# Optimization experiments

Measured on AMD Instinct MI355X. Metric: run time of the kernel, lower is better.

Reference implementation:

```python
import jax, jax.numpy as jnp
import numpy as np

N, E, IN, H, HEADS, L, OUT = 4096, 262144, 64, 128, 4, 2, 2
DH = H // HEADS  # 32, per-head dim for both GAT and global MHA
BN_EPS = 1e-5
NEG_SLOPE = 0.2  # GATConv leaky_relu default


def setup_inputs() -> dict:
    key = jax.random.key(0)
    ks = iter(jax.random.split(key, 32))
    rn = lambda shape, s: jax.random.normal(next(ks), shape, jnp.float32) * s
    return {
        "x": rn((N, IN), 1.0),
        "edge_index": jax.random.randint(next(ks), (2, E), 0, N),
        "w_in": rn((H, IN), IN ** -0.5),
        "b_in": rn((H,), 0.02),
        "w_gat": rn((L, H, H), H ** -0.5),
        "att_src": rn((L, HEADS, DH), 0.1),
        "att_dst": rn((L, HEADS, DH), 0.1),
        "b_gat": rn((L, H), 0.02),
        "w_qkv": rn((L, 3 * H, H), H ** -0.5),
        "b_qkv": rn((L, 3 * H), 0.02),
        "w_o": rn((L, H, H), H ** -0.5),
        "b_o": rn((L, H), 0.02),
        "bn_gamma": 1.0 + rn((L, 3, H), 0.05),
        "bn_beta": rn((L, 3, H), 0.05),
        "w1": rn((L, 2 * H, H), H ** -0.5),
        "b1": rn((L, 2 * H), 0.02),
        "w2": rn((L, H, 2 * H), (2 * H) ** -0.5),
        "b2": rn((L, H), 0.02),
        "w_out": rn((OUT, H), H ** -0.5),
        "b_out": rn((OUT,), 0.02),
    }


def _bn(h, g, b):
    # eval-mode BatchNorm1d with running_mean=0, running_var=1
    return h * (g / jnp.sqrt(1.0 + BN_EPS)) + b


def _gat(x, src, dst, w, a_src, a_dst, bias):
    # GATConv(hidden, hidden//heads, heads=HEADS, add_self_loops=False), concat=True
    xp = (x @ w.T).reshape(N, HEADS, DH)                  # [N, HEADS, DH]
    al_s = jnp.einsum('nhd,hd->nh', xp, a_src)            # [N, HEADS]
    al_d = jnp.einsum('nhd,hd->nh', xp, a_dst)
    logit = al_s[src] + al_d[dst]                         # [E, HEADS]
    logit = jnp.where(logit >= 0, logit, NEG_SLOPE * logit)
    m = jax.ops.segment_max(logit, dst, num_segments=N)   # scatter-softmax over dst
    m = jnp.where(jnp.isfinite(m), m, 0.0)
    e = jnp.exp(logit - m[dst])
    denom = jax.ops.segment_sum(e, dst, num_segments=N)
    alpha = e / (denom[dst] + 1e-16)
    out = jax.ops.segment_sum(alpha[:, :, None] * xp[src], dst, num_segments=N)
    return out.reshape(N, H) + bias


def _mha(x, wqkv, bqkv, wo, bo):
    # torch.nn.MultiheadAttention self-attention over all N nodes (one graph)
    qkv = x @ wqkv.T + bqkv
    q, k, v = jnp.split(qkv, 3, axis=-1)
    q = q.reshape(N, HEADS, DH)
    k = k.reshape(N, HEADS, DH)
    v = v.reshape(N, HEADS, DH)
    scores = jnp.einsum('nhd,mhd->hnm', q, k) / jnp.sqrt(jnp.float32(DH))
    attn = jax.nn.softmax(scores, axis=-1)
    out = jnp.einsum('hnm,mhd->nhd', attn, v).reshape(N, H)
    return out @ wo.T + bo


def reference(x, edge_index, w_in, b_in, w_gat, att_src, att_dst, b_gat,
              w_qkv, b_qkv, w_o, b_o, bn_gamma, bn_beta,
              w1, b1, w2, b2, w_out, b_out):
    src, dst = edge_index[0], edge_index[1]
    h = jax.nn.relu(x @ w_in.T + b_in)
    for l in range(L):
        # GPSConv: local GAT branch (dropout inactive in eval)
        h_loc = _gat(h, src, dst, w_gat[l], att_src[l], att_dst[l], b_gat[l]) + h
        h_loc = _bn(h_loc, bn_gamma[l, 0], bn_beta[l, 0])
        # GPSConv: global attention branch
        h_att = _mha(h, w_qkv[l], b_qkv[l], w_o[l], b_o[l]) + h
        h_att = _bn(h_att, bn_gamma[l, 1], bn_beta[l, 1])
        out = h_loc + h_att
        mlp = jax.nn.relu(out @ w1[l].T + b1[l]) @ w2[l].T + b2[l]
        out = _bn(out + mlp, bn_gamma[l, 2], bn_beta[l, 2])
        # GPSRiskModel residual + relu (dropout inactive in eval)
        h = jax.nn.relu(out + h)
    return h @ w_out.T + b_out
```

## Files before the change

### kernel.cpp

```cpp
#include <hip/hip_runtime.h>

#define NN 4096
#define EE 262144
#define INF_ 64
#define HH 128
#define HEADS 4
#define DH 32
#define LL 2
#define NH (NN * HH)
#define KSPLIT 16
#define L2E 1.4426950408889634f

typedef unsigned short u16;
typedef unsigned int u32;
using bf16x8 = __attribute__((ext_vector_type(8))) short;
using f32x4 = __attribute__((ext_vector_type(4))) float;

__device__ __forceinline__ float bf2f(u16 v) { return __uint_as_float(((u32)v) << 16); }
__device__ __forceinline__ u16 f2bf(float f) {
    u32 u = __float_as_uint(f);
    u32 r = (u + 0x7fffu + ((u >> 16) & 1u)) >> 16;
    return (u16)r;
}
__device__ __forceinline__ u32 encf(float f) {
    u32 b = __float_as_uint(f);
    return (b & 0x80000000u) ? ~b : (b | 0x80000000u);
}
__device__ __forceinline__ float decf(u32 u) {
    u32 b = (u & 0x80000000u) ? (u & 0x7fffffffu) : ~u;
    return __uint_as_float(b);
}

__global__ __launch_bounds__(256) void k_detect(const u16* __restrict__ x, int* __restrict__ flag,
                                                int* __restrict__ cnt, u32* __restrict__ gmax) {
    int t = threadIdx.x;
    for (int i = t; i < NN; i += 256) cnt[i] = 0;
    if (t < 16) gmax[t] = 0;
    __shared__ int cs[256];
    u16 v = x[2 * t];
    int e = (v >> 7) & 0xFF;
    cs[t] = (e >= 100 && e <= 140) ? 1 : 0;
    __syncthreads();
    for (int s = 128; s > 0; s >>= 1) {
        if (t < s) cs[t] += cs[t + s];
        __syncthreads();
    }
    if (t == 0) *flag = (cs[0] >= 128) ? 1 : 0;
}

#define MAXSEG 16
struct SegF { const void* src[MAXSEG]; int dst[MAXSEG]; int n[MAXSEG]; int cnt; };
__global__ void k_cvtf(SegF S, float* __restrict__ W, const int* __restrict__ flag) {
    int seg = blockIdx.y;
    if (seg >= S.cnt) return;
    int n = S.n[seg];
    float* d = W + S.dst[seg];
    const void* s = S.src[seg];
    int f = *flag;
    for (int i = blockIdx.x * 256 + threadIdx.x; i < n; i += gridDim.x * 256)
        d[i] = f ? bf2f(((const u16*)s)[i]) : ((const float*)s)[i];
}
struct SegB { const void* src[8]; u16* dst[8]; u16* dst2[8]; int n[8]; int cnt; };
__global__ void k_cvtb(SegB S, const int* __restrict__ flag) {
    int seg = blockIdx.y;
    if (seg >= S.cnt) return;
    int f = *flag;
    u16* d = S.dst[seg];
    u16* d2 = S.dst2[seg];
    if (f && !d2) return;
    int n = S.n[seg];
    const void* s = S.src[seg];
    for (int i = blockIdx.x * 256 + threadIdx.x; i < n; i += gridDim.x * 256) {
        if (d2) {
            float v = f ? bf2f(((const u16*)s)[i]) : ((const float*)s)[i];
            u16 h = f2bf(v);
            d[i] = h;
            d2[i] = f2bf(v - bf2f(h));
        } else {
            d[i] = f2bf(((const float*)s)[i]);
        }
    }
}

__global__ void k_hist(const int* __restrict__ dst, int* __restrict__ cnt) {
    int e = blockIdx.x * blockDim.x + threadIdx.x;
    if (e < EE) atomicAdd(&cnt[dst[e]], 1);
}
__global__ __launch_bounds__(256) void k_scan(const int* __restrict__ cnt, int* __restrict__ rowstart,
                                              int* __restrict__ cursor) {
    __shared__ int part[256];
    int t = threadIdx.x;
    int loc[16];
    int s = 0;
#pragma unroll
    for (int i = 0; i < 16; ++i) { loc[i] = s; s += cnt[t * 16 + i]; }
    part[t] = s;
    __syncthreads();
    for (int off = 1; off < 256; off <<= 1) {
        int v = part[t];
        int a = (t >= off) ? part[t - off] : 0;
        __syncthreads();
        part[t] = v + a;
        __syncthreads();
    }
    int base = (t == 0) ? 0 : part[t - 1];
#pragma unroll
    for (int i = 0; i < 16; ++i) {
        rowstart[t * 16 + i] = base + loc[i];
        cursor[t * 16 + i] = base + loc[i];
    }
}
__global__ void k_scatter(const int* __restrict__ src, const int* __restrict__ dst,
                          int* __restrict__ cursor, int* __restrict__ esrc) {
    int e = blockIdx.x * blockDim.x + threadIdx.x;
    if (e < EE) {
        int d = dst[e];
        int p = atomicAdd(&cursor[d], 1);
        esrc[p] = src[e];
    }
}

__global__ __launch_bounds__(128) void k_mgemm(const u16* __restrict__ Ahi, const u16* __restrict__ Alo,
                                               const u16* __restrict__ Wc, const u16* __restrict__ Wd,
                                               const int* __restrict__ flag,
                                               const float* __restrict__ bias,
                                               float* __restrict__ outf, u16* __restrict__ outb16,
                                               u16* __restrict__ outhi, u16* __restrict__ outlo,
                                               int K, int J, int relu) {
    const u16* Wb = (*flag) ? Wd : Wc;
    int wave = threadIdx.x >> 6, lane = threadIdx.x & 63;
    int grp = lane >> 4, lcol = lane & 15;
    int m0 = blockIdx.x * 32 + wave * 16;
    int j0 = blockIdx.y * 64;
    f32x4 acc[4];
#pragma unroll
    for (int s = 0; s < 4; ++s) acc[s] = (f32x4){0.f, 0.f, 0.f, 0.f};
    const u16* ah = Ahi + (size_t)(m0 + lcol) * K + grp * 8;
    const u16* al = Alo + (size_t)(m0 + lcol) * K + grp * 8;
    const u16* wb = Wb + (size_t)(j0 + lcol) * K + grp * 8;
    for (int k = 0; k < K; k += 32) {
        bf16x8 va = *(const bf16x8*)(ah + k);
        bf16x8 vl = *(const bf16x8*)(al + k);
#pragma unroll
        for (int s = 0; s < 4; ++s) {
            bf16x8 vw = *(const bf16x8*)(wb + (size_t)s * 16 * K + k);
            acc[s] = __builtin_amdgcn_mfma_f32_16x16x32_bf16(va, vw, acc[s], 0, 0, 0);
            acc[s] = __builtin_amdgcn_mfma_f32_16x16x32_bf16(vl, vw, acc[s], 0, 0, 0);
        }
    }
#pragma unroll
    for (int s = 0; s < 4; ++s) {
        int col = j0 + s * 16 + lcol;
        float bs = bias ? bias[col] : 0.f;
#pragma unroll
        for (int r = 0; r < 4; ++r) {
            float v = acc[s][r] + bs;
            if (relu) v = fmaxf(v, 0.f);
            size_t idx = (size_t)(m0 + grp * 4 + r) * J + col;
            if (outf) outf[idx] = v;
            if (outb16) outb16[idx] = f2bf(v);
            if (outhi) {
                u16 hv = f2bf(v);
                outhi[idx] = hv;
                outlo[idx] = f2bf(v - bf2f(hv));
            }
        }
    }
}

__global__ __launch_bounds__(128) void k_gemm_gq(const u16* __restrict__ Ahi, const u16* __restrict__ Alo,
                                                 const u16* __restrict__ wgatc, const u16* __restrict__ wgatd,
                                                 const u16* __restrict__ wqkvc, const u16* __restrict__ wqkvd,
                                                 const int* __restrict__ flag,
                                                 const float* __restrict__ bqkv,
                                                 u16* __restrict__ xpb, u16* __restrict__ qkvb) {
    int wave = threadIdx.x >> 6, lane = threadIdx.x & 63;
    int grp = lane >> 4, lcol = lane & 15;
    int m0 = blockIdx.x * 32 + wave * 16;
    int jb = blockIdx.y;
    int j0 = jb * 64;
    int f = *flag;
    const u16* wgat = f ? wgatd : wgatc;
    const u16* wqkv = f ? wqkvd : wqkvc;
    const u16* Wb = (jb < 2) ? (wgat + (size_t)j0 * HH) : (wqkv + (size_t)(j0 - 128) * HH);
    f32x4 acc[4];
#pragma unroll
    for (int s = 0; s < 4; ++s) acc[s] = (f32x4){0.f, 0.f, 0.f, 0.f};
    const u16* ah = Ahi + (size_t)(m0 + lcol) * HH + grp * 8;
    const u16* al = Alo + (size_t)(m0 + lcol) * HH + grp * 8;
    const u16* wb = Wb + (size_t)lcol * HH + grp * 8;
    for (int k = 0; k < HH; k += 32) {
        bf16x8 va = *(const bf16x8*)(ah + k);
        bf16x8 vl = *(const bf16x8*)(al + k);
#pragma unroll
        for (int s = 0; s < 4; ++s) {
            bf16x8 vw = *(const bf16x8*)(wb + (size_t)s * 16 * HH + k);
            acc[s] = __builtin_amdgcn_mfma_f32_16x16x32_bf16(va, vw, acc[s], 0, 0, 0);
            acc[s] = __builtin_amdgcn_mfma_f32_16x16x32_bf16(vl, vw, acc[s], 0, 0, 0);
        }
    }
    if (jb < 2) {
#pragma unroll
        for (int s = 0; s < 4; ++s) {
            int col = j0 + s * 16 + lcol;
#pragma unroll
            for (int r = 0; r < 4; ++r)
                xpb[(size_t)(m0 + grp * 4 + r) * HH + col] = f2bf(acc[s][r]);
        }
    } else {
#pragma unroll
        for (int s = 0; s < 4; ++s) {
            int colq = j0 - 128 + s * 16 + lcol;
            float bs = bqkv[colq];
#pragma unroll
            for (int r = 0; r < 4; ++r)
                qkvb[(size_t)(m0 + grp * 4 + r) * 384 + colq] = f2bf(acc[s][r] + bs);
        }
    }
}

__global__ __launch_bounds__(256) void k_attlog(const u16* __restrict__ xpb, const float* __restrict__ asrc,
                                                const float* __restrict__ adst, float* __restrict__ als,
                                                float* __restrict__ ald, u32* __restrict__ gmax) {
    int t = blockIdx.x * 256 + threadIdx.x;
    int n = t >> 2, hh = t & 3;
    const u16* xr = xpb + (size_t)n * HH + hh * DH;
    float s1 = 0.f, s2 = 0.f;
#pragma unroll
    for (int d = 0; d < DH; ++d) {
        float v = bf2f(xr[d]);
        s1 += v * asrc[hh * DH + d];
        s2 += v * adst[hh * DH + d];
    }
    als[t] = s1;
    ald[t] = s2;
    __shared__ float red[256];
    int lt = threadIdx.x;
    red[lt] = s1;
    __syncthreads();
    for (int off = 128; off >= 4; off >>= 1) {
        if (lt < off) red[lt] = fmaxf(red[lt], red[lt + off]);
        __syncthreads();
    }
    if (lt < 4) atomicMax(&gmax[lt], encf(red[lt]));
    __syncthreads();
    red[lt] = s2;
    __syncthreads();
    for (int off = 128; off >= 4; off >>= 1) {
        if (lt < off) red[lt] = fmaxf(red[lt], red[lt + off]);
        __syncthreads();
    }
    if (lt < 4) atomicMax(&gmax[4 + lt], encf(red[lt]));
}

__global__ __launch_bounds__(128) void k_gemm_wo(const u16* __restrict__ Ahi, const u16* __restrict__ Alo,
                                                 const u16* __restrict__ Wc, const u16* __restrict__ Wd,
                                                 const int* __restrict__ flag,
                                                 const float* __restrict__ bias,
                                                 const float* __restrict__ gatb, const float* __restrict__ hbuf,
                                                 const float* __restrict__ bgat, const float* __restrict__ gam,
                                                 const float* __restrict__ bet,
                                                 float* __restrict__ outb, u16* __restrict__ ohi,
                                                 u16* __restrict__ olo) {
    const u16* Wb = (*flag) ? Wd : Wc;
    int wave = threadIdx.x >> 6, lane = threadIdx.x & 63;
    int grp = lane >> 4, lcol = lane & 15;
    int m0 = blockIdx.x * 32 + wave * 16;
    int j0 = blockIdx.y * 64;
    f32x4 acc[4];
#pragma unroll
    for (int s = 0; s < 4; ++s) acc[s] = (f32x4){0.f, 0.f, 0.f, 0.f};
    const u16* ah = Ahi + (size_t)(m0 + lcol) * HH + grp * 8;
    const u16* al = Alo + (size_t)(m0 + lcol) * HH + grp * 8;
    const u16* wb = Wb + (size_t)(j0 + lcol) * HH + grp * 8;
    for (int k = 0; k < HH; k += 32) {
        bf16x8 va = *(const bf16x8*)(ah + k);
        bf16x8 vl = *(const bf16x8*)(al + k);
#pragma unroll
        for (int s = 0; s < 4; ++s) {
            bf16x8 vw = *(const bf16x8*)(wb + (size_t)s * 16 * HH + k);
            acc[s] = __builtin_amdgcn_mfma_f32_16x16x32_bf16(va, vw, acc[s], 0, 0, 0);
            acc[s] = __builtin_amdgcn_mfma_f32_16x16x32_bf16(vl, vw, acc[s], 0, 0, 0);
        }
    }
    float rs = rsqrtf(1.00001f);
#pragma unroll
    for (int s = 0; s < 4; ++s) {
        int col = j0 + s * 16 + lcol;
        float bs = bias[col];
        float g0 = gam[col] * rs, b0 = bet[col];
        float g1 = gam[HH + col] * rs, b1 = bet[HH + col];
        float bg = bgat[col];
#pragma unroll
        for (int r = 0; r < 4; ++r) {
            size_t idx = (size_t)(m0 + grp * 4 + r) * HH + col;
            float proj = acc[s][r] + bs;
            float hv = hbuf[idx];
            float hl = g0 * (gatb[idx] + bg + hv) + b0;
            float ha = g1 * (proj + hv) + b1;
            float v = hl + ha;
            outb[idx] = v;
            u16 hb = f2bf(v);
            ohi[idx] = hb;
            olo[idx] = f2bf(v - bf2f(hb));
        }
    }
}

__global__ __launch_bounds__(128) void k_gemm_w2(const u16* __restrict__ Ahi, const u16* __restrict__ Alo,
                                                 const u16* __restrict__ Wc, const u16* __restrict__ Wd,
                                                 const int* __restrict__ flag,
                                                 const float* __restrict__ bias,
                                                 const float* __restrict__ outb, const float* __restrict__ gam2,
                                                 const float* __restrict__ bet2,
                                                 float* __restrict__ hbuf, u16* __restrict__ hhi,
                                                 u16* __restrict__ hlo) {
    const u16* Wb = (*flag) ? Wd : Wc;
    int wave = threadIdx.x >> 6, lane = threadIdx.x & 63;
    int grp = lane >> 4, lcol = lane & 15;
    int m0 = blockIdx.x * 32 + wave * 16;
    int j0 = blockIdx.y * 64;
    const int K = 2 * HH;
    f32x4 acc[4];
#pragma unroll
    for (int s = 0; s < 4; ++s) acc[s] = (f32x4){0.f, 0.f, 0.f, 0.f};
    const u16* ah = Ahi + (size_t)(m0 + lcol) * K + grp * 8;
    const u16* al = Alo + (size_t)(m0 + lcol) * K + grp * 8;
    const u16* wb = Wb + (size_t)(j0 + lcol) * K + grp * 8;
    for (int k = 0; k < K; k += 32) {
        bf16x8 va = *(const bf16x8*)(ah + k);
        bf16x8 vl = *(const bf16x8*)(al + k);
#pragma unroll
        for (int s = 0; s < 4; ++s) {
            bf16x8 vw = *(const bf16x8*)(wb + (size_t)s * 16 * K + k);
            acc[s] = __builtin_amdgcn_mfma_f32_16x16x32_bf16(va, vw, acc[s], 0, 0, 0);
            acc[s] = __builtin_amdgcn_mfma_f32_16x16x32_bf16(vl, vw, acc[s], 0, 0, 0);
        }
    }
    float rs = rsqrtf(1.00001f);
#pragma unroll
    for (int s = 0; s < 4; ++s) {
        int col = j0 + s * 16 + lcol;
        float bs = bias[col];
        float g2 = gam2[col] * rs, b2 = bet2[col];
#pragma unroll
        for (int r = 0; r < 4; ++r) {
            size_t idx = (size_t)(m0 + grp * 4 + r) * HH + col;
            float mlpo = acc[s][r] + bs;
            float o2 = g2 * (outb[idx] + mlpo) + b2;
            float v = fmaxf(o2 + hbuf[idx], 0.f);
            hbuf[idx] = v;
            u16 hb = f2bf(v);
            hhi[idx] = hb;
            hlo[idx] = f2bf(v - bf2f(hb));
        }
    }
}

#define GCHUNK 256
__global__ __launch_bounds__(128) void k_gat_node(const int* __restrict__ esrc, const int* __restrict__ rowstart,
                                                  const int* __restrict__ cnt, const float* __restrict__ als,
                                                  const float* __restrict__ ald, const u16* __restrict__ xpb,
                                                  float* __restrict__ gatout, const u32* __restrict__ gmax) {
    int n = blockIdx.x, t = threadIdx.x;
    int base = rowstart[n], c = cnt[n];
    float4 adv = ((const float4*)ald)[n];
    float ad[4] = {adv.x, adv.y, adv.z, adv.w};
    float M2[4];
#pragma unroll
    for (int h = 0; h < 4; ++h) {
        float bound = decf(gmax[h]) + decf(gmax[4 + h]);
        float M = bound >= 0.f ? bound : 0.2f * bound;
        M2[h] = M * L2E;
    }
    __shared__ float red[512];
    __shared__ float elds[GCHUNK * 4];
    __shared__ int slds[GCHUNK];
    float dsum[4] = {0.f, 0.f, 0.f, 0.f};
    float acc = 0.f;
    int ht = t >> 5;
    for (int ch = 0; ch < c; ch += GCHUNK) {
        int cn = min(GCHUNK, c - ch);
        __syncthreads();
        for (int i = t; i < cn; i += 128) {
            int s = esrc[base + ch + i];
            slds[i] = s;
            float4 as = ((const float4*)als)[s];
            float lg, e;
            lg = as.x + ad[0]; lg = lg >= 0.f ? lg : 0.2f * lg; e = __builtin_exp2f(lg * L2E - M2[0]); elds[i * 4 + 0] = e; dsum[0] += e;
            lg = as.y + ad[1]; lg = lg >= 0.f ? lg : 0.2f * lg; e = __builtin_exp2f(lg * L2E - M2[1]); elds[i * 4 + 1] = e; dsum[1] += e;
            lg = as.z + ad[2]; lg = lg >= 0.f ? lg : 0.2f * lg; e = __builtin_exp2f(lg * L2E - M2[2]); elds[i * 4 + 2] = e; dsum[2] += e;
            lg = as.w + ad[3]; lg = lg >= 0.f ? lg : 0.2f * lg; e = __builtin_exp2f(lg * L2E - M2[3]); elds[i * 4 + 3] = e; dsum[3] += e;
        }
        __syncthreads();
        int i = 0;
        for (; i + 4 <= cn; i += 4) {
            int s0 = slds[i], s1 = slds[i + 1], s2 = slds[i + 2], s3 = slds[i + 3];
            float x0 = bf2f(xpb[(size_t)s0 * HH + t]);
            float x1 = bf2f(xpb[(size_t)s1 * HH + t]);
            float x2 = bf2f(xpb[(size_t)s2 * HH + t]);
            float x3 = bf2f(xpb[(size_t)s3 * HH + t]);
            acc += elds[i * 4 + ht] * x0 + elds[(i + 1) * 4 + ht] * x1;
            acc += elds[(i + 2) * 4 + ht] * x2 + elds[(i + 3) * 4 + ht] * x3;
        }
        for (; i < cn; ++i) acc += elds[i * 4 + ht] * bf2f(xpb[(size_t)slds[i] * HH + t]);
    }
    __syncthreads();
#pragma unroll
    for (int h = 0; h < 4; ++h) red[h * 128 + t] = dsum[h];
    __syncthreads();
    for (int s2 = 64; s2 > 0; s2 >>= 1) {
        if (t < s2) {
#pragma unroll
            for (int h = 0; h < 4; ++h)
                red[h * 128 + t] += red[h * 128 + t + s2];
        }
        __syncthreads();
    }
    float inv = 1.f / (red[ht * 128] + 1e-16f);
    gatout[(size_t)n * HH + t] = acc * inv;
}

__global__ __launch_bounds__(256) void k_mha_split(const u16* __restrict__ qkvb,
                                                   float* __restrict__ PM, float* __restrict__ PL,
                                                   u16* __restrict__ PO) {
    const float C1 = 0.17677669529663687f * L2E;
    int head = blockIdx.x & 3;
    int qt = (blockIdx.x >> 2) & 31;
    int ks = blockIdx.x >> 7;
    int tid = threadIdx.x;
    int wave = tid >> 6, lane = tid & 63;
    int grp = lane >> 4, lcol = lane & 15;

    __shared__ __align__(16) u16 Klds[64][40];
    __shared__ __align__(16) u32 Vlds[32][40];
    __shared__ __align__(16) u16 Plds[4][32][36];

    int qrow0 = qt * 128 + wave * 32;
    bf16x8 aQ0 = *(const bf16x8*)(qkvb + (size_t)(qrow0 + lcol) * 384 + head * 32 + grp * 8);
    bf16x8 aQ1 = *(const bf16x8*)(qkvb + (size_t)(qrow0 + 16 + lcol) * 384 + head * 32 + grp * 8);

    short onev = (lcol == 0) ? (short)0x3F80 : (short)0;
    bf16x8 bOne = {onev, onev, onev, onev, onev, onev, onev, onev};

    f32x4 oc00 = {0.f, 0.f, 0.f, 0.f}, oc01 = {0.f, 0.f, 0.f, 0.f};
    f32x4 oc10 = {0.f, 0.f, 0.f, 0.f}, oc11 = {0.f, 0.f, 0.f, 0.f};
    f32x4 ol0 = {0.f, 0.f, 0.f, 0.f}, ol1 = {0.f, 0.f, 0.f, 0.f};
    float msh = -INFINITY;

    int isK = (tid < 128);
    int st = tid & 127;
    int skey = st >> 1, shalf = (st & 1) * 16;
    int vj = st & 15, vc = (st >> 4) & 1, dgrp = st >> 5;
    const u16* kptr = qkvb + 128 + head * 32 + shalf;
    const u16* vptr = qkvb + 256 + head * 32 + dgrp * 8;
    int vk0 = vc * 32 + vj;
    int vk1 = vc * 32 + 16 + vj;

    int kt0 = ks * (NN / KSPLIT);
    bf16x8 r0, r1;
    if (isK) {
        r0 = *(const bf16x8*)(kptr + (size_t)(kt0 + skey) * 384);
        r1 = *(const bf16x8*)(kptr + (size_t)(kt0 + skey) * 384 + 8);
    } else {
        r0 = *(const bf16x8*)(vptr + (size_t)(kt0 + vk0) * 384);
        r1 = *(const bf16x8*)(vptr + (size_t)(kt0 + vk1) * 384);
    }

    const int NT = (NN / KSPLIT) / 64;
    for (int t = 0; t < NT; ++t) {
        if (isK) {
            *(bf16x8*)(&Klds[skey][shalf]) = r0;
            *(bf16x8*)(&Klds[skey][shalf + 8]) = r1;
        } else {
#pragma unroll
            for (int j = 0; j < 8; ++j)
                Vlds[dgrp * 8 + j][vc * 20 + vj] = (u32)(u16)r0[j] | ((u32)(u16)r1[j] << 16);
        }
        __syncthreads();
        if (t + 1 < NT) {
            int kn = kt0 + (t + 1) * 64;
            if (isK) {
                r0 = *(const bf16x8*)(kptr + (size_t)(kn + skey) * 384);
                r1 = *(const bf16x8*)(kptr + (size_t)(kn + skey) * 384 + 8);
            } else {
                r0 = *(const bf16x8*)(vptr + (size_t)(kn + vk0) * 384);
                r1 = *(const bf16x8*)(vptr + (size_t)(kn + vk1) * 384);
            }
        }
        f32x4 sc0[4], sc1[4];
        f32x4 zero = {0.f, 0.f, 0.f, 0.f};
#pragma unroll
        for (int s = 0; s < 4; ++s) {
            bf16x8 bK = *(const bf16x8*)(&Klds[s * 16 + lcol][grp * 8]);
            sc0[s] = __builtin_amdgcn_mfma_f32_16x16x32_bf16(aQ0, bK, zero, 0, 0, 0);
            sc1[s] = __builtin_amdgcn_mfma_f32_16x16x32_bf16(aQ1, bK, zero, 0, 0, 0);
        }
        float mymax = sc0[0][0];
#pragma unroll
        for (int s = 0; s < 4; ++s)
#pragma unroll
            for (int r = 0; r < 4; ++r) {
                mymax = fmaxf(mymax, sc0[s][r]);
                mymax = fmaxf(mymax, sc1[s][r]);
            }
        mymax = fmaxf(mymax, __shfl_xor(mymax, 1));
        mymax = fmaxf(mymax, __shfl_xor(mymax, 2));
        mymax = fmaxf(mymax, __shfl_xor(mymax, 4));
        mymax = fmaxf(mymax, __shfl_xor(mymax, 8));
        float mnew = fmaxf(msh, mymax * C1);
        float cc = __builtin_exp2f(msh - mnew);
        msh = mnew;
        oc00 *= cc; oc01 *= cc; ol0 *= cc;
        oc10 *= cc; oc11 *= cc; ol1 *= cc;
#pragma unroll
        for (int c2 = 0; c2 < 2; ++c2) {
#pragma unroll
            for (int r = 0; r < 4; ++r) {
                float p0 = __builtin_exp2f(__builtin_fmaf(sc0[2 * c2][r], C1, -mnew));
                float p1 = __builtin_exp2f(__builtin_fmaf(sc0[2 * c2 + 1][r], C1, -mnew));
                *(u32*)(&Plds[wave][grp * 4 + r][2 * lcol]) =
                    __builtin_amdgcn_perm(__float_as_uint(p1), __float_as_uint(p0), 0x07060302u);
                float q0 = __builtin_exp2f(__builtin_fmaf(sc1[2 * c2][r], C1, -mnew));
                float q1 = __builtin_exp2f(__builtin_fmaf(sc1[2 * c2 + 1][r], C1, -mnew));
                *(u32*)(&Plds[wave][16 + grp * 4 + r][2 * lcol]) =
                    __builtin_amdgcn_perm(__float_as_uint(q1), __float_as_uint(q0), 0x07060302u);
            }
            bf16x8 aP0 = *(const bf16x8*)(&Plds[wave][lcol][grp * 8]);
            bf16x8 aP1 = *(const bf16x8*)(&Plds[wave][16 + lcol][grp * 8]);
            bf16x8 bV0 = *(const bf16x8*)(&Vlds[lcol][c2 * 20 + grp * 4]);
            bf16x8 bV1 = *(const bf16x8*)(&Vlds[16 + lcol][c2 * 20 + grp * 4]);
            oc00 = __builtin_amdgcn_mfma_f32_16x16x32_bf16(aP0, bV0, oc00, 0, 0, 0);
            oc01 = __builtin_amdgcn_mfma_f32_16x16x32_bf16(aP0, bV1, oc01, 0, 0, 0);
            ol0 = __builtin_amdgcn_mfma_f32_16x16x32_bf16(aP0, bOne, ol0, 0, 0, 0);
            oc10 = __builtin_amdgcn_mfma_f32_16x16x32_bf16(aP1, bV0, oc10, 0, 0, 0);
            oc11 = __builtin_amdgcn_mfma_f32_16x16x32_bf16(aP1, bV1, oc11, 0, 0, 0);
            ol1 = __builtin_amdgcn_mfma_f32_16x16x32_bf16(aP1, bOne, ol1, 0, 0, 0);
        }
        __syncthreads();
    }
#pragma unroll
    for (int r = 0; r < 4; ++r) {
        int row0 = qrow0 + grp * 4 + r;
        size_t b0 = ((size_t)row0 * HEADS + head) * KSPLIT + ks;
        PO[b0 * 32 + lcol] = f2bf(oc00[r]);
        PO[b0 * 32 + 16 + lcol] = f2bf(oc01[r]);
        int row1 = row0 + 16;
        size_t b1 = ((size_t)row1 * HEADS + head) * KSPLIT + ks;
        PO[b1 * 32 + lcol] = f2bf(oc10[r]);
        PO[b1 * 32 + 16 + lcol] = f2bf(oc11[r]);
        if (lcol == 0) {
            PM[b0] = msh;
            PL[b0] = ol0[r];
            PM[b1] = msh;
            PL[b1] = ol1[r];
        }
    }
}

__global__ __launch_bounds__(256) void k_mha_comb(const float* __restrict__ PM, const float* __restrict__ PL,
                                                  const u16* __restrict__ PO, u16* __restrict__ atthi,
                                                  u16* __restrict__ attlo) {
    __shared__ float wn[2][4][KSPLIT];
    int row0 = blockIdx.x * 2;
    int t = threadIdx.x;
    if (t < 2 * 4 * KSPLIT) {
        int rr = t >> 6, head = (t >> 4) & 3, ks = t & 15;
        size_t b = ((size_t)(row0 + rr) * HEADS + head) * KSPLIT + ks;
        float pm = PM[b];
        float m = pm;
#pragma unroll
        for (int off = 1; off < 16; off <<= 1) m = fmaxf(m, __shfl_xor(m, off));
        float w = __builtin_exp2f(pm - m);
        float lw = PL[b] * w;
#pragma unroll
        for (int off = 1; off < 16; off <<= 1) lw += __shfl_xor(lw, off);
        wn[rr][head][ks] = w / lw;
    }
    __syncthreads();
    int rr = t >> 7, col = t & 127;
    int head = col >> 5, dim = col & 31;
    int row = row0 + rr;
    size_t b0 = ((size_t)row * HEADS + head) * KSPLIT;
    float o = 0.f;
#pragma unroll
    for (int k = 0; k < KSPLIT; ++k)
        o += wn[rr][head][k] * bf2f(PO[(b0 + k) * 32 + dim]);
    size_t idx = (size_t)row * HH + col;
    u16 h = f2bf(o);
    atthi[idx] = h;
    attlo[idx] = f2bf(o - bf2f(h));
}

__global__ __launch_bounds__(64) void k_out(const float* __restrict__ h, const float* __restrict__ w,
                                            const float* __restrict__ b, void* __restrict__ yout,
                                            const int* __restrict__ flag) {
    int n = blockIdx.x, l = threadIdx.x;
    float a0 = 0.f, a1 = 0.f;
    for (int k = l; k < HH; k += 64) {
        float hv = h[(size_t)n * HH + k];
        a0 += hv * w[k];
        a1 += hv * w[HH + k];
    }
#pragma unroll
    for (int off = 32; off > 0; off >>= 1) {
        a0 += __shfl_xor(a0, off);
        a1 += __shfl_xor(a1, off);
    }
    if (l == 0) {
        float o0 = a0 + b[0], o1 = a1 + b[1];
        if (*flag) {
            u16* y = (u16*)yout;
            y[n * 2 + 0] = f2bf(o0);
            y[n * 2 + 1] = f2bf(o1);
        } else {
            float* y = (float*)yout;
            y[n * 2 + 0] = o0;
            y[n * 2 + 1] = o1;
        }
    }
}

extern "C" void kernel_launch(void* const* d_in, const int* in_sizes, int n_in,
                              void* d_out, int out_size, void* d_ws, size_t ws_size,
                              hipStream_t stream) {
    float* W = (float*)d_ws;
    size_t o = 0;
    auto take = [&](size_t n) { size_t r = o; o += n; return r; };
    size_t pb_in = take(HH);
    size_t pattS = take(LL * HEADS * DH);
    size_t pattD = take(LL * HEADS * DH);
    size_t pb_gat = take(LL * HH);
    size_t pb_qkv = take(LL * 3 * HH);
    size_t pb_o  = take(LL * HH);
    size_t pbn_g = take(LL * 3 * HH);
    size_t pbn_b = take(LL * 3 * HH);
    size_t pb1   = take(LL * 2 * HH);
    size_t pb2   = take(LL * HH);
    size_t pw_out = take(2 * HH);
    size_t pb_out = take(2);
    auto takeb = [&](size_t nu16) { size_t r = o; o += (nu16 + 1) / 2; return r; };
    size_t bw_in  = takeb(HH * INF_);
    size_t bw_gat = takeb(LL * HH * HH);
    size_t bw_qkv = takeb(LL * 3 * HH * HH);
    size_t bw_o   = takeb(LL * HH * HH);
    size_t bw1    = takeb(LL * 2 * HH * HH);
    size_t bw2    = takeb(LL * HH * 2 * HH);
    o = (o + 127) & ~(size_t)127;
    size_t ohbuf = take(NH);
    size_t ogat  = take(NH);
    size_t otmp  = take(NH);
    size_t oals  = take(NN * HEADS);
    size_t oald  = take(NN * HEADS);
    size_t opm   = take(NN * HEADS * KSPLIT);
    size_t opl   = take(NN * HEADS * KSPLIT);
    size_t opo   = takeb((size_t)NN * HEADS * KSPLIT * 32);
    size_t oqkvb = takeb(NN * 384);
    size_t oxpb  = takeb(NH);
    size_t oxhi  = takeb(NN * INF_);
    size_t oxlo  = takeb(NN * INF_);
    size_t ohhi  = takeb(NH);
    size_t ohlo  = takeb(NH);
    size_t oahi  = takeb(NH);
    size_t oalo  = takeb(NH);
    size_t oohi  = takeb(NH);
    size_t oolo  = takeb(NH);
    size_t omhi  = takeb(NN * 2 * HH);
    size_t omlo  = takeb(NN * 2 * HH);
    int* ibase    = (int*)(W + o);
    int* iflag    = ibase;
    int* cnt      = ibase + 64;
    int* rowstart = cnt + NN;
    int* cursor   = rowstart + NN;
    int* esrc     = cursor + NN;
    u32* gmax     = (u32*)(esrc + EE);

    float* hbuf = W + ohbuf;
    float* gatb = W + ogat;
    float* tmp  = W + otmp;
    float* als  = W + oals;
    float* ald  = W + oald;
    float* pmb  = W + opm;
    float* plb  = W + opl;
    u16* pob  = (u16*)(W + opo);
    u16* qkvb = (u16*)(W + oqkvb);
    u16* xpb  = (u16*)(W + oxpb);
    u16* xhi = (u16*)(W + oxhi), *xlo = (u16*)(W + oxlo);
    u16* hhi = (u16*)(W + ohhi), *hlo = (u16*)(W + ohlo);
    u16* ahi = (u16*)(W + oahi), *alo = (u16*)(W + oalo);
    u16* ohi = (u16*)(W + oohi), *olo = (u16*)(W + oolo);
    u16* mhi = (u16*)(W + omhi), *mlo = (u16*)(W + omlo);

    const int* src = (const int*)d_in[1];
    const int* dst = (const int*)d_in[1] + EE;
    const u16* dw_in  = (const u16*)d_in[2];
    const u16* dw_gat = (const u16*)d_in[4];
    const u16* dw_qkv = (const u16*)d_in[8];
    const u16* dw_o   = (const u16*)d_in[10];
    const u16* dw1    = (const u16*)d_in[14];
    const u16* dw2    = (const u16*)d_in[16];

    k_detect<<<1, 256, 0, stream>>>((const u16*)d_in[0], iflag, cnt, gmax);

    SegF SF = {};
    int nf = 0;
    auto addf = [&](int idx, size_t off, int n) { SF.src[nf] = d_in[idx]; SF.dst[nf] = (int)off; SF.n[nf] = n; ++nf; };
    addf(3, pb_in, HH);
    addf(5, pattS, LL * HEADS * DH);
    addf(6, pattD, LL * HEADS * DH);
    addf(7, pb_gat, LL * HH);
    addf(9, pb_qkv, LL * 3 * HH);
    addf(11, pb_o, LL * HH);
    addf(12, pbn_g, LL * 3 * HH);
    addf(13, pbn_b, LL * 3 * HH);
    addf(15, pb1, LL * 2 * HH);
    addf(17, pb2, LL * HH);
    addf(18, pw_out, 2 * HH);
    addf(19, pb_out, 2);
    SF.cnt = nf;
    k_cvtf<<<dim3(8, nf), 256, 0, stream>>>(SF, W, iflag);

    SegB SB = {};
    int nb = 0;
    auto addb = [&](int idx, size_t off, int n, u16* d2) {
        SB.src[nb] = d_in[idx]; SB.dst[nb] = (u16*)(W + off); SB.dst2[nb] = d2; SB.n[nb] = n; ++nb;
    };
    addb(2, bw_in, HH * INF_, nullptr);
    addb(4, bw_gat, LL * HH * HH, nullptr);
    addb(8, bw_qkv, LL * 3 * HH * HH, nullptr);
    addb(10, bw_o, LL * HH * HH, nullptr);
    addb(14, bw1, LL * 2 * HH * HH, nullptr);
    addb(16, bw2, LL * HH * 2 * HH, nullptr);
    SB.src[nb] = d_in[0]; SB.dst[nb] = xhi; SB.dst2[nb] = xlo; SB.n[nb] = NN * INF_; ++nb;
    SB.cnt = nb;
    k_cvtb<<<dim3(128, nb), 256, 0, stream>>>(SB, iflag);

    k_hist<<<EE / 256, 256, 0, stream>>>(dst, cnt);
    k_scan<<<1, 256, 0, stream>>>(cnt, rowstart, cursor);
    k_scatter<<<EE / 256, 256, 0, stream>>>(src, dst, cursor, esrc);

    k_mgemm<<<dim3(NN / 32, HH / 64), 128, 0, stream>>>(xhi, xlo, (u16*)(W + bw_in), dw_in, iflag,
                                                        W + pb_in, hbuf, nullptr, hhi, hlo, INF_, HH, 1);

    for (int l = 0; l < LL; ++l) {
        k_gemm_gq<<<dim3(NN / 32, 8), 128, 0, stream>>>(hhi, hlo,
                                                        (u16*)(W + bw_gat) + (size_t)l * HH * HH,
                                                        dw_gat + (size_t)l * HH * HH,
                                                        (u16*)(W + bw_qkv) + (size_t)l * 3 * HH * HH,
                                                        dw_qkv + (size_t)l * 3 * HH * HH,
                                                        iflag, W + pb_qkv + l * 3 * HH, xpb, qkvb);
        k_attlog<<<(NN * HEADS) / 256, 256, 0, stream>>>(xpb, W + pattS + l * HEADS * DH,
                                                         W + pattD + l * HEADS * DH, als, ald,
                                                         gmax + l * 8);
        k_gat_node<<<NN, 128, 0, stream>>>(esrc, rowstart, cnt, als, ald, xpb, gatb, gmax + l * 8);
        k_mha_split<<<(NN / 128) * HEADS * KSPLIT, 256, 0, stream>>>(qkvb, pmb, plb, pob);
        k_mha_comb<<<NN / 2, 256, 0, stream>>>(pmb, plb, pob, ahi, alo);
        k_gemm_wo<<<dim3(NN / 32, HH / 64), 128, 0, stream>>>(ahi, alo,
                                                              (u16*)(W + bw_o) + (size_t)l * HH * HH,
                                                              dw_o + (size_t)l * HH * HH, iflag,
                                                              W + pb_o + l * HH, gatb, hbuf,
                                                              W + pb_gat + l * HH, W + pbn_g + l * 3 * HH,
                                                              W + pbn_b + l * 3 * HH, tmp, ohi, olo);
        k_mgemm<<<dim3(NN / 32, 256 / 64), 128, 0, stream>>>(ohi, olo,
                                                             (u16*)(W + bw1) + (size_t)l * 2 * HH * HH,
                                                             dw1 + (size_t)l * 2 * HH * HH, iflag,
                                                             W + pb1 + l * 2 * HH, nullptr, nullptr,
                                                             mhi, mlo, HH, 2 * HH, 1);
        k_gemm_w2<<<dim3(NN / 32, HH / 64), 128, 0, stream>>>(mhi, mlo,
                                                              (u16*)(W + bw2) + (size_t)l * HH * 2 * HH,
                                                              dw2 + (size_t)l * HH * 2 * HH, iflag,
                                                              W + pb2 + l * HH, tmp,
                                                              W + pbn_g + l * 3 * HH + 2 * HH,
                                                              W + pbn_b + l * 3 * HH + 2 * HH,
                                                              hbuf, hhi, hlo);
    }
    k_out<<<NN, 64, 0, stream>>>(hbuf, W + pw_out, W + pb_out, d_out, iflag);
}
```

Measured before the change: 321.2 us.

## Merge independent kernels via block-range dispatch to cut launch count

Merges independent kernels into single launches that pick their role from the block index. The weight conversion and edge histogram become one prep kernel. The attention-logit computation rides along with the MHA split kernel, and the GAT node aggregation shares a launch with the MHA combine. The aim is to remove several launches per layer and let independent work overlap on the GPU. In exchange, the merged kernels carry the shared-memory footprint and register pressure of their larger member, which may lower occupancy for the lighter parts.

```diff
diff --git a/kernel.cpp b/kernel.cpp
--- a/kernel.cpp
+++ b/kernel.cpp
@@ -50,42 +50,46 @@
 
 #define MAXSEG 16
 struct SegF { const void* src[MAXSEG]; int dst[MAXSEG]; int n[MAXSEG]; int cnt; };
-__global__ void k_cvtf(SegF S, float* __restrict__ W, const int* __restrict__ flag) {
-    int seg = blockIdx.y;
-    if (seg >= S.cnt) return;
-    int n = S.n[seg];
-    float* d = W + S.dst[seg];
-    const void* s = S.src[seg];
-    int f = *flag;
-    for (int i = blockIdx.x * 256 + threadIdx.x; i < n; i += gridDim.x * 256)
-        d[i] = f ? bf2f(((const u16*)s)[i]) : ((const float*)s)[i];
-}
 struct SegB { const void* src[8]; u16* dst[8]; u16* dst2[8]; int n[8]; int cnt; };
-__global__ void k_cvtb(SegB S, const int* __restrict__ flag) {
-    int seg = blockIdx.y;
-    if (seg >= S.cnt) return;
-    int f = *flag;
-    u16* d = S.dst[seg];
-    u16* d2 = S.dst2[seg];
-    if (f && !d2) return;
-    int n = S.n[seg];
-    const void* s = S.src[seg];
-    for (int i = blockIdx.x * 256 + threadIdx.x; i < n; i += gridDim.x * 256) {
-        if (d2) {
-            float v = f ? bf2f(((const u16*)s)[i]) : ((const float*)s)[i];
-            u16 h = f2bf(v);
-            d[i] = h;
-            d2[i] = f2bf(v - bf2f(h));
-        } else {
-            d[i] = f2bf(((const float*)s)[i]);
-        }
-    }
-}
-
-__global__ void k_hist(const int* __restrict__ dst, int* __restrict__ cnt) {
-    int e = blockIdx.x * blockDim.x + threadIdx.x;
-    if (e < EE) atomicAdd(&cnt[dst[e]], 1);
-}
+__global__ __launch_bounds__(256) void k_prep(SegF SF, float* __restrict__ W, SegB SB,
+                                              const int* __restrict__ flag,
+                                              const int* __restrict__ dst, int* __restrict__ cnt) {
+    int bid = blockIdx.x, t = threadIdx.x;
+    if (bid < 96) {
+        int seg = bid >> 3, bx = bid & 7;
+        if (seg >= SF.cnt) return;
+        int n = SF.n[seg];
+        float* d = W + SF.dst[seg];
+        const void* s = SF.src[seg];
+        int f = *flag;
+        for (int i = bx * 256 + t; i < n; i += 8 * 256)
+            d[i] = f ? bf2f(((const u16*)s)[i]) : ((const float*)s)[i];
+    } else if (bid < 992) {
+        int b2 = bid - 96;
+        int seg = b2 >> 7, bx = b2 & 127;
+        if (seg >= SB.cnt) return;
+        int f = *flag;
+        u16* d = SB.dst[seg];
+        u16* d2 = SB.dst2[seg];
+        if (f && !d2) return;
+        int n = SB.n[seg];
+        const void* s = SB.src[seg];
+        for (int i = bx * 256 + t; i < n; i += 128 * 256) {
+            if (d2) {
+                float v = f ? bf2f(((const u16*)s)[i]) : ((const float*)s)[i];
+                u16 h = f2bf(v);
+                d[i] = h;
+                d2[i] = f2bf(v - bf2f(h));
+            } else {
+                d[i] = f2bf(((const float*)s)[i]);
+            }
+        }
+    } else {
+        int e = (bid - 992) * 256 + t;
+        if (e < EE) atomicAdd(&cnt[dst[e]], 1);
+    }
+}
+
 __global__ __launch_bounds__(256) void k_scan(const int* __restrict__ cnt, int* __restrict__ rowstart,
                                               int* __restrict__ cursor) {
     __shared__ int part[256];
@@ -219,40 +223,6 @@
     }
 }
 
-__global__ __launch_bounds__(256) void k_attlog(const u16* __restrict__ xpb, const float* __restrict__ asrc,
-                                                const float* __restrict__ adst, float* __restrict__ als,
-                                                float* __restrict__ ald, u32* __restrict__ gmax) {
-    int t = blockIdx.x * 256 + threadIdx.x;
-    int n = t >> 2, hh = t & 3;
-    const u16* xr = xpb + (size_t)n * HH + hh * DH;
-    float s1 = 0.f, s2 = 0.f;
-#pragma unroll
-    for (int d = 0; d < DH; ++d) {
-        float v = bf2f(xr[d]);
-        s1 += v * asrc[hh * DH + d];
-        s2 += v * adst[hh * DH + d];
-    }
-    als[t] = s1;
-    ald[t] = s2;
-    __shared__ float red[256];
-    int lt = threadIdx.x;
-    red[lt] = s1;
-    __syncthreads();
-    for (int off = 128; off >= 4; off >>= 1) {
-        if (lt < off) red[lt] = fmaxf(red[lt], red[lt + off]);
-        __syncthreads();
-    }
-    if (lt < 4) atomicMax(&gmax[lt], encf(red[lt]));
-    __syncthreads();
-    red[lt] = s2;
-    __syncthreads();
-    for (int off = 128; off >= 4; off >>= 1) {
-        if (lt < off) red[lt] = fmaxf(red[lt], red[lt + off]);
-        __syncthreads();
-    }
-    if (lt < 4) atomicMax(&gmax[4 + lt], encf(red[lt]));
-}
-
 __global__ __launch_bounds__(128) void k_gemm_wo(const u16* __restrict__ Ahi, const u16* __restrict__ Alo,
                                                  const u16* __restrict__ Wc, const u16* __restrict__ Wd,
                                                  const int* __restrict__ flag,
@@ -357,73 +327,51 @@
     }
 }
 
-#define GCHUNK 256
-__global__ __launch_bounds__(128) void k_gat_node(const int* __restrict__ esrc, const int* __restrict__ rowstart,
-                                                  const int* __restrict__ cnt, const float* __restrict__ als,
-                                                  const float* __restrict__ ald, const u16* __restrict__ xpb,
-                                                  float* __restrict__ gatout, const u32* __restrict__ gmax) {
-    int n = blockIdx.x, t = threadIdx.x;
-    int base = rowstart[n], c = cnt[n];
-    float4 adv = ((const float4*)ald)[n];
-    float ad[4] = {adv.x, adv.y, adv.z, adv.w};
-    float M2[4];
-#pragma unroll
-    for (int h = 0; h < 4; ++h) {
-        float bound = decf(gmax[h]) + decf(gmax[4 + h]);
-        float M = bound >= 0.f ? bound : 0.2f * bound;
-        M2[h] = M * L2E;
-    }
-    __shared__ float red[512];
-    __shared__ float elds[GCHUNK * 4];
-    __shared__ int slds[GCHUNK];
-    float dsum[4] = {0.f, 0.f, 0.f, 0.f};
-    float acc = 0.f;
-    int ht = t >> 5;
-    for (int ch = 0; ch < c; ch += GCHUNK) {
-        int cn = min(GCHUNK, c - ch);
-        __syncthreads();
-        for (int i = t; i < cn; i += 128) {
-            int s = esrc[base + ch + i];
-            slds[i] = s;
-            float4 as = ((const float4*)als)[s];
-            float lg, e;
-            lg = as.x + ad[0]; lg = lg >= 0.f ? lg : 0.2f * lg; e = __builtin_exp2f(lg * L2E - M2[0]); elds[i * 4 + 0] = e; dsum[0] += e;
-            lg = as.y + ad[1]; lg = lg >= 0.f ? lg : 0.2f * lg; e = __builtin_exp2f(lg * L2E - M2[1]); elds[i * 4 + 1] = e; dsum[1] += e;
-            lg = as.z + ad[2]; lg = lg >= 0.f ? lg : 0.2f * lg; e = __builtin_exp2f(lg * L2E - M2[2]); elds[i * 4 + 2] = e; dsum[2] += e;
-            lg = as.w + ad[3]; lg = lg >= 0.f ? lg : 0.2f * lg; e = __builtin_exp2f(lg * L2E - M2[3]); elds[i * 4 + 3] = e; dsum[3] += e;
-        }
-        __syncthreads();
-        int i = 0;
-        for (; i + 4 <= cn; i += 4) {
-            int s0 = slds[i], s1 = slds[i + 1], s2 = slds[i + 2], s3 = slds[i + 3];
-            float x0 = bf2f(xpb[(size_t)s0 * HH + t]);
-            float x1 = bf2f(xpb[(size_t)s1 * HH + t]);
-            float x2 = bf2f(xpb[(size_t)s2 * HH + t]);
-            float x3 = bf2f(xpb[(size_t)s3 * HH + t]);
-            acc += elds[i * 4 + ht] * x0 + elds[(i + 1) * 4 + ht] * x1;
-            acc += elds[(i + 2) * 4 + ht] * x2 + elds[(i + 3) * 4 + ht] * x3;
-        }
-        for (; i < cn; ++i) acc += elds[i * 4 + ht] * bf2f(xpb[(size_t)slds[i] * HH + t]);
-    }
-    __syncthreads();
-#pragma unroll
-    for (int h = 0; h < 4; ++h) red[h * 128 + t] = dsum[h];
-    __syncthreads();
-    for (int s2 = 64; s2 > 0; s2 >>= 1) {
-        if (t < s2) {
-#pragma unroll
-            for (int h = 0; h < 4; ++h)
-                red[h * 128 + t] += red[h * 128 + t + s2];
-        }
-        __syncthreads();
-    }
-    float inv = 1.f / (red[ht * 128] + 1e-16f);
-    gatout[(size_t)n * HH + t] = acc * inv;
-}
-
-__global__ __launch_bounds__(256) void k_mha_split(const u16* __restrict__ qkvb,
-                                                   float* __restrict__ PM, float* __restrict__ PL,
-                                                   u16* __restrict__ PO) {
+__global__ __launch_bounds__(256) void k_splitlog(const u16* __restrict__ qkvb,
+                                                  float* __restrict__ PM, float* __restrict__ PL,
+                                                  u16* __restrict__ PO,
+                                                  const u16* __restrict__ xpb,
+                                                  const float* __restrict__ asrc,
+                                                  const float* __restrict__ adst,
+                                                  float* __restrict__ als, float* __restrict__ ald,
+                                                  u32* __restrict__ gmax) {
+    __shared__ __align__(16) u16 Klds[64][40];
+    __shared__ __align__(16) u32 Vlds[32][40];
+    __shared__ __align__(16) u16 Plds[4][32][36];
+
+    if (blockIdx.x >= 2048) {
+        float* red = (float*)&Klds[0][0];
+        int t = (blockIdx.x - 2048) * 256 + threadIdx.x;
+        int n = t >> 2, hh = t & 3;
+        const u16* xr = xpb + (size_t)n * HH + hh * DH;
+        float s1 = 0.f, s2 = 0.f;
+#pragma unroll
+        for (int d = 0; d < DH; ++d) {
+            float v = bf2f(xr[d]);
+            s1 += v * asrc[hh * DH + d];
+            s2 += v * adst[hh * DH + d];
+        }
+        als[t] = s1;
+        ald[t] = s2;
+        int lt = threadIdx.x;
+        red[lt] = s1;
+        __syncthreads();
+        for (int off = 128; off >= 4; off >>= 1) {
+            if (lt < off) red[lt] = fmaxf(red[lt], red[lt + off]);
+            __syncthreads();
+        }
+        if (lt < 4) atomicMax(&gmax[lt], encf(red[lt]));
+        __syncthreads();
+        red[lt] = s2;
+        __syncthreads();
+        for (int off = 128; off >= 4; off >>= 1) {
+            if (lt < off) red[lt] = fmaxf(red[lt], red[lt + off]);
+            __syncthreads();
+        }
+        if (lt < 4) atomicMax(&gmax[4 + lt], encf(red[lt]));
+        return;
+    }
+
     const float C1 = 0.17677669529663687f * L2E;
     int head = blockIdx.x & 3;
     int qt = (blockIdx.x >> 2) & 31;
@@ -431,10 +379,6 @@
     int tid = threadIdx.x;
     int wave = tid >> 6, lane = tid & 63;
     int grp = lane >> 4, lcol = lane & 15;
-
-    __shared__ __align__(16) u16 Klds[64][40];
-    __shared__ __align__(16) u32 Vlds[32][40];
-    __shared__ __align__(16) u16 Plds[4][32][36];
 
     int qrow0 = qt * 128 + wave * 32;
     bf16x8 aQ0 = *(const bf16x8*)(qkvb + (size_t)(qrow0 + lcol) * 384 + head * 32 + grp * 8);
@@ -558,38 +502,103 @@
     }
 }
 
-__global__ __launch_bounds__(256) void k_mha_comb(const float* __restrict__ PM, const float* __restrict__ PL,
-                                                  const u16* __restrict__ PO, u16* __restrict__ atthi,
-                                                  u16* __restrict__ attlo) {
-    __shared__ float wn[2][4][KSPLIT];
-    int row0 = blockIdx.x * 2;
+#define GCHUNK 256
+__global__ __launch_bounds__(128) void k_gatcomb(const int* __restrict__ esrc, const int* __restrict__ rowstart,
+                                                 const int* __restrict__ cnt, const float* __restrict__ als,
+                                                 const float* __restrict__ ald, const u16* __restrict__ xpb,
+                                                 float* __restrict__ gatout, const u32* __restrict__ gmax,
+                                                 const float* __restrict__ PM, const float* __restrict__ PL,
+                                                 const u16* __restrict__ PO, u16* __restrict__ atthi,
+                                                 u16* __restrict__ attlo) {
+    __shared__ float red[512];
+    __shared__ float elds[GCHUNK * 4];
+    __shared__ int slds[GCHUNK];
     int t = threadIdx.x;
-    if (t < 2 * 4 * KSPLIT) {
-        int rr = t >> 6, head = (t >> 4) & 3, ks = t & 15;
-        size_t b = ((size_t)(row0 + rr) * HEADS + head) * KSPLIT + ks;
-        float pm = PM[b];
-        float m = pm;
-#pragma unroll
-        for (int off = 1; off < 16; off <<= 1) m = fmaxf(m, __shfl_xor(m, off));
-        float w = __builtin_exp2f(pm - m);
-        float lw = PL[b] * w;
-#pragma unroll
-        for (int off = 1; off < 16; off <<= 1) lw += __shfl_xor(lw, off);
-        wn[rr][head][ks] = w / lw;
+
+    if (blockIdx.x >= NN) {
+        int n2 = blockIdx.x - NN;
+        float* wn = red;
+        if (t < 64) {
+            int head = t >> 4, ks = t & 15;
+            size_t b = ((size_t)n2 * HEADS + head) * KSPLIT + ks;
+            float pm = PM[b];
+            float m = pm;
+#pragma unroll
+            for (int off = 1; off < 16; off <<= 1) m = fmaxf(m, __shfl_xor(m, off));
+            float w = __builtin_exp2f(pm - m);
+            float lw = PL[b] * w;
+#pragma unroll
+            for (int off = 1; off < 16; off <<= 1) lw += __shfl_xor(lw, off);
+            wn[t] = w / lw;
+        }
+        __syncthreads();
+        int head = t >> 5, dim = t & 31;
+        size_t b0 = ((size_t)n2 * HEADS + head) * KSPLIT;
+        float o = 0.f;
+#pragma unroll
+        for (int k = 0; k < KSPLIT; ++k)
+            o += wn[head * 16 + k] * bf2f(PO[(b0 + k) * 32 + dim]);
+        size_t idx = (size_t)n2 * HH + t;
+        u16 h = f2bf(o);
+        atthi[idx] = h;
+        attlo[idx] = f2bf(o - bf2f(h));
+        return;
+    }
+
+    int n = blockIdx.x;
+    int base = rowstart[n], c = cnt[n];
+    float4 adv = ((const float4*)ald)[n];
+    float ad[4] = {adv.x, adv.y, adv.z, adv.w};
+    float M2[4];
+#pragma unroll
+    for (int h = 0; h < 4; ++h) {
+        float bound = decf(gmax[h]) + decf(gmax[4 + h]);
+        float M = bound >= 0.f ? bound : 0.2f * bound;
+        M2[h] = M * L2E;
+    }
+    float dsum[4] = {0.f, 0.f, 0.f, 0.f};
+    float acc = 0.f;
+    int ht = t >> 5;
+    for (int ch = 0; ch < c; ch += GCHUNK) {
+        int cn = min(GCHUNK, c - ch);
+        __syncthreads();
+        for (int i = t; i < cn; i += 128) {
+            int s = esrc[base + ch + i];
+            slds[i] = s;
+            float4 as = ((const float4*)als)[s];
+            float lg, e;
+            lg = as.x + ad[0]; lg = lg >= 0.f ? lg : 0.2f * lg; e = __builtin_exp2f(lg * L2E - M2[0]); elds[i * 4 + 0] = e; dsum[0] += e;
+            lg = as.y + ad[1]; lg = lg >= 0.f ? lg : 0.2f * lg; e = __builtin_exp2f(lg * L2E - M2[1]); elds[i * 4 + 1] = e; dsum[1] += e;
+            lg = as.z + ad[2]; lg = lg >= 0.f ? lg : 0.2f * lg; e = __builtin_exp2f(lg * L2E - M2[2]); elds[i * 4 + 2] = e; dsum[2] += e;
+            lg = as.w + ad[3]; lg = lg >= 0.f ? lg : 0.2f * lg; e = __builtin_exp2f(lg * L2E - M2[3]); elds[i * 4 + 3] = e; dsum[3] += e;
+        }
+        __syncthreads();
+        int i = 0;
+        for (; i + 4 <= cn; i += 4) {
+            int s0 = slds[i], s1 = slds[i + 1], s2 = slds[i + 2], s3 = slds[i + 3];
+            float x0 = bf2f(xpb[(size_t)s0 * HH + t]);
+            float x1 = bf2f(xpb[(size_t)s1 * HH + t]);
+            float x2 = bf2f(xpb[(size_t)s2 * HH + t]);
+            float x3 = bf2f(xpb[(size_t)s3 * HH + t]);
+            acc += elds[i * 4 + ht] * x0 + elds[(i + 1) * 4 + ht] * x1;
+            acc += elds[(i + 2) * 4 + ht] * x2 + elds[(i + 3) * 4 + ht] * x3;
+        }
+        for (; i < cn; ++i) acc += elds[i * 4 + ht] * bf2f(xpb[(size_t)slds[i] * HH + t]);
     }
     __syncthreads();
-    int rr = t >> 7, col = t & 127;
-    int head = col >> 5, dim = col & 31;
-    int row = row0 + rr;
-    size_t b0 = ((size_t)row * HEADS + head) * KSPLIT;
-    float o = 0.f;
-#pragma unroll
-    for (int k = 0; k < KSPLIT; ++k)
-        o += wn[rr][head][k] * bf2f(PO[(b0 + k) * 32 + dim]);
-    size_t idx = (size_t)row * HH + col;
-    u16 h = f2bf(o);
-    atthi[idx] = h;
-    attlo[idx] = f2bf(o - bf2f(h));
+#pragma unroll
+    for (int h = 0; h < 4; ++h) red[h * 128 + t] = dsum[h];
+    __syncthreads();
+    for (int s2 = 64; s2 > 0; s2 >>= 1) {
+        if (t < s2) {
+#pragma unroll
+            for (int h = 0; h < 4; ++h)
+                red[h * 128 + t] += red[h * 128 + t + s2];
+        }
+        __syncthreads();
+    }
+    float inv = 1.f / (red[ht * 128] + 1e-16f);
+    gatout[(size_t)n * HH + t] = acc * inv;
 }
 
 __global__ __launch_bounds__(64) void k_out(const float* __restrict__ h, const float* __restrict__ w,
@@ -718,7 +727,6 @@
     addf(18, pw_out, 2 * HH);
     addf(19, pb_out, 2);
     SF.cnt = nf;
-    k_cvtf<<<dim3(8, nf), 256, 0, stream>>>(SF, W, iflag);
 
     SegB SB = {};
     int nb = 0;
@@ -733,9 +741,9 @@
     addb(16, bw2, LL * HH * 2 * HH, nullptr);
     SB.src[nb] = d_in[0]; SB.dst[nb] = xhi; SB.dst2[nb] = xlo; SB.n[nb] = NN * INF_; ++nb;
     SB.cnt = nb;
-    k_cvtb<<<dim3(128, nb), 256, 0, stream>>>(SB, iflag);
-
-    k_hist<<<EE / 256, 256, 0, stream>>>(dst, cnt);
+
+    k_prep<<<2016, 256, 0, stream>>>(SF, W, SB, iflag, dst, cnt);
+
     k_scan<<<1, 256, 0, stream>>>(cnt, rowstart, cursor);
     k_scatter<<<EE / 256, 256, 0, stream>>>(src, dst, cursor, esrc);
 
@@ -749,12 +757,12 @@
                                                         (u16*)(W + bw_qkv) + (size_t)l * 3 * HH * HH,
                                                         dw_qkv + (size_t)l * 3 * HH * HH,
                                                         iflag, W + pb_qkv + l * 3 * HH, xpb, qkvb);
-        k_attlog<<<(NN * HEADS) / 256, 256, 0, stream>>>(xpb, W + pattS + l * HEADS * DH,
-                                                         W + pattD + l * HEADS * DH, als, ald,
-                                                         gmax + l * 8);
-        k_gat_node<<<NN, 128, 0, stream>>>(esrc, rowstart, cnt, als, ald, xpb, gatb, gmax + l * 8);
-        k_mha_split<<<(NN / 128) * HEADS * KSPLIT, 256, 0, stream>>>(qkvb, pmb, plb, pob);
-        k_mha_comb<<<NN / 2, 256, 0, stream>>>(pmb, plb, pob, ahi, alo);
+        k_splitlog<<<2048 + (NN * HEADS) / 256, 256, 0, stream>>>(qkvb, pmb, plb, pob, xpb,
+                                                                  W + pattS + l * HEADS * DH,
+                                                                  W + pattD + l * HEADS * DH,
+                                                                  als, ald, gmax + l * 8);
+        k_gatcomb<<<2 * NN, 128, 0, stream>>>(esrc, rowstart, cnt, als, ald, xpb, gatb, gmax + l * 8,
+                                              pmb, plb, pob, ahi, alo);
         k_gemm_wo<<<dim3(NN / 32, HH / 64), 128, 0, stream>>>(ahi, alo,
                                                               (u16*)(W + bw_o) + (size_t)l * HH * HH,
                                                               dw_o + (size_t)l * HH * HH, iflag,
```

Result: faster. 296.3 us (-7.7%).
